# Optimization experiments

Hardware: AMD Instinct MI355X
Metric: run time of the kernel (lower is better)

## Reference

```python
import jax, jax.numpy as jnp
import numpy as np

B, L, H, S2V = 32, 1024, 256, 256
STEP = 1          # HP_SLSTM_step window size
EPS = 1e-3        # LayerNorm eps (added to std, torch-style unbiased std)
NUM_LAYERS = 4
# LayerNorm param row indices in ln_a/ln_b:
# 0..5 -> word gates f1,f2,f3,f4,i,o ; 6 gd ; 7 go ; 8 gf ; 9 gi ; 10 gg


def _ln(x, a, b):
    # torch LayerNorm variant: unbiased std, eps added to std (not var)
    mean = x.mean(-1, keepdims=True)
    d = x - mean
    std = jnp.sqrt((d * d).sum(-1, keepdims=True) / (x.shape[-1] - 1))
    return a * d / (std + EPS) + b


def setup_inputs() -> dict:
    key = jax.random.key(0)
    ks = jax.random.split(key, 16)
    p = lambda k, shp: 0.1 * jax.random.normal(k, shp, dtype=jnp.float32)
    return {
        "word_inputs": jax.random.normal(ks[0], (B, L, H), dtype=jnp.float32),
        "sent_embeddings": jax.random.normal(ks[1], (B, S2V), dtype=jnp.float32),
        "mask": jnp.ones((B, L), dtype=jnp.float32),
        "h0": jax.random.uniform(ks[2], (B, L, H), minval=-0.05, maxval=0.05, dtype=jnp.float32),
        "c0": jax.random.uniform(ks[3], (B, L, H), minval=-0.05, maxval=0.05, dtype=jnp.float32),
        "Wx_g": p(ks[4], (6, H, H)),
        "Wh_g": p(ks[5], (6, 2 * H, H)),
        "Wi_g": p(ks[6], (6, H, H)),
        "Wd_g": p(ks[7], (6, H, H)),
        "b_g": p(ks[8], (6, H)),
        "gWx": p(ks[9], (4, H, H)),   # dummy gates d,i,o,f
        "gWh": p(ks[10], (4, H, H)),
        "gWg": p(ks[11], (4, S2V, H)),  # d,i,o,g
        "gb": p(ks[12], (4, H)),
        "ln_a": jnp.ones((11, H), dtype=jnp.float32),
        "ln_b": jnp.zeros((11, H), dtype=jnp.float32),
        "num_layers": NUM_LAYERS,
    }


def _win_sums(t):
    # sum of left-shifted (before) and right-shifted (after) neighbor states
    bef = jnp.zeros_like(t)
    aft = jnp.zeros_like(t)
    for s in range(1, STEP + 1):
        bef = bef + jnp.pad(t[:, :-s], ((0, 0), (s, 0), (0, 0)))
        aft = aft + jnp.pad(t[:, s:], ((0, 0), (0, s), (0, 0)))
    return bef.reshape(-1, t.shape[-1]), aft.reshape(-1, t.shape[-1])


def reference(word_inputs, sent_embeddings, mask, h0, c0, Wx_g, Wh_g, Wi_g,
              Wd_g, b_g, gWx, gWh, gWg, gb, ln_a, ln_b, num_layers):
    Bs, Ls, Hs = word_inputs.shape
    seq_mask = mask[..., None]                      # (B,L,1)
    msm = (mask * 1e25 - 1e25)[..., None]           # softmax mask (B,L,1)
    emb_h = (word_inputs * seq_mask).reshape(-1, Hs)  # fixed word embedding states
    emb_c = emb_h
    h = h0 * seq_mask
    c = c0 * seq_mask
    dh = h.mean(axis=1)                             # dummy (sentence) node (B,H)
    dc = c.mean(axis=1)

    for _ in range(num_layers):
        comb = h.mean(axis=1)                       # (B,H)
        rh = h.reshape(-1, Hs)                      # (B*L,H)
        tdh = (dh[:, None, :] * seq_mask).reshape(-1, Hs)
        tdc = (dc[:, None, :] * seq_mask).reshape(-1, Hs)

        # --- dummy (sentence-level) node gates ---
        gd = jax.nn.sigmoid(_ln(dh @ gWx[0] + sent_embeddings @ gWg[0] + comb @ gWh[0] + gb[0], ln_a[6], ln_b[6]))
        gi = jax.nn.sigmoid(_ln(dh @ gWx[1] + sent_embeddings @ gWg[1] + comb @ gWh[1], ln_a[9], ln_b[9]) + gb[1])  # bias outside LN, as in source
        gg = sent_embeddings @ gWg[3]
        go = jax.nn.sigmoid(_ln(dh @ gWx[2] + sent_embeddings @ gWg[2] + comb @ gWh[2] + gb[2], ln_a[7], ln_b[7]))
        gf = jax.nn.sigmoid(_ln(tdh @ gWx[3] + rh @ gWh[3] + gb[3], ln_a[8], ln_b[8]))
        gf = gf.reshape(Bs, Ls, Hs) + msm
        scores = jax.nn.softmax(jnp.concatenate([gf, gd[:, None, :], gi[:, None, :]], axis=1), axis=1)
        f_w = scores[:, :Ls]
        d_w = scores[:, Ls]
        i_w = scores[:, Ls + 1]
        dc_new = jnp.sum(f_w * c, axis=1) + d_w * dc + i_w * jnp.tanh(_ln(gg, ln_a[10], ln_b[10]))
        dh_new = go * jnp.tanh(dc_new)

        # --- word node gates (windowed message passing) ---
        hb, ha = _win_sums(h)
        cb, ca = _win_sums(c)
        cat_h = jnp.concatenate([hb, ha], axis=1)   # (B*L, 2H)
        pre = (jnp.einsum('nh,ghk->gnk', emb_h, Wx_g)
               + jnp.einsum('nc,gck->gnk', cat_h, Wh_g)
               + jnp.einsum('nh,ghk->gnk', rh, Wi_g)
               + jnp.einsum('nh,ghk->gnk', tdh, Wd_g)
               + b_g[:, None, :])                   # (6, B*L, H)
        gates = jax.nn.sigmoid(_ln(pre, ln_a[:6, None, :], ln_b[:6, None, :]))
        five = jax.nn.softmax(gates[:5], axis=0)    # normalize f1..f4,i
        f1, f2, f3, f4, i_t = five
        o_t = gates[5]
        c_new = cb * f1 + ca * f2 + emb_c * f3 + tdc * f4 + c.reshape(-1, Hs) * i_t
        h_new = o_t * jnp.tanh(c_new)
        h = h_new.reshape(Bs, Ls, Hs) * seq_mask
        c = c_new.reshape(Bs, Ls, Hs) * seq_mask
        dh, dc = dh_new, dc_new
    return h
```

## Files before the change

### kernel.cpp

```cpp
#include <hip/hip_runtime.h>
#include <cstddef>

#define Bz 32
#define Lz 1024
#define Hz 256
#define Nz (Bz*Lz)
#define NHz ((size_t)Nz*Hz)
#define BHz (Bz*Hz)
#define EPSz 1e-3f
#define NLAYERS 4
#define NCH 64
#define NTC 112
#define CHR 16384

typedef __bf16 bf8_t __attribute__((ext_vector_type(8)));
typedef __bf16 bf4_t __attribute__((ext_vector_type(4)));
typedef float  f4_t  __attribute__((ext_vector_type(4)));

__device__ inline float sigmoidf(float x){ return 1.f/(1.f+expf(-x)); }
__device__ inline float fsig(float x){ return __builtin_amdgcn_rcpf(1.f + __expf(-x)); }
__device__ inline float ftanh(float x){ return 1.f - 2.f*__builtin_amdgcn_rcpf(__expf(2.f*x)+1.f); }

template<int C>
__device__ inline float dppadd(float v){
  int t = __builtin_amdgcn_update_dpp(0, __builtin_bit_cast(int, v), C, 0xf, 0xf, true);
  return v + __builtin_bit_cast(float, t);
}
__device__ inline float dppsum16(float v){
  v = dppadd<0x111>(v);
  v = dppadd<0x112>(v);
  v = dppadd<0x114>(v);
  v = dppadd<0x118>(v);
  return v;
}

__device__ inline void gl_lds16(const void* g, void* l){
  __builtin_amdgcn_global_load_lds(
      (const __attribute__((address_space(1))) void*)g,
      (__attribute__((address_space(3))) void*)l, 16, 0, 0);
}

__device__ inline float2 block_sum2(float a, float b, float* red){
  #pragma unroll
  for (int off=32; off; off>>=1){ a += __shfl_down(a,off,64); b += __shfl_down(b,off,64); }
  int w = threadIdx.x>>6;
  __syncthreads();
  if ((threadIdx.x&63)==0){ red[w]=a; red[4+w]=b; }
  __syncthreads();
  return make_float2(red[0]+red[1]+red[2]+red[3], red[4]+red[5]+red[6]+red[7]);
}

__device__ inline float ln_block(float v, const float* la, const float* lb, int t, float* red){
  float2 ss = block_sum2(v, v*v, red);
  float mean = ss.x*(1.f/Hz);
  float var  = (ss.y - (float)Hz*mean*mean)*(1.f/(Hz-1));
  float isd  = 1.f/(sqrtf(fmaxf(var,0.f))+EPSz);
  return la[t]*(v-mean)*isd + lb[t];
}

__global__ void k_initb(const float* __restrict__ word, const float* __restrict__ h0,
                        const float* __restrict__ c0, const float* __restrict__ mask,
                        __bf16* __restrict__ xe, __bf16* __restrict__ h, __bf16* __restrict__ c){
  int tid = blockIdx.x*256 + threadIdx.x;
  int n = tid >> 5; int c8 = (tid & 31)*8;
  float m = mask[n];
  size_t off = (size_t)n*Hz + c8;
  const float4* wv = (const float4*)(word + off);
  float4 w0 = wv[0], w1 = wv[1];
  bf8_t o;
  o[0]=(__bf16)(w0.x*m); o[1]=(__bf16)(w0.y*m); o[2]=(__bf16)(w0.z*m); o[3]=(__bf16)(w0.w*m);
  o[4]=(__bf16)(w1.x*m); o[5]=(__bf16)(w1.y*m); o[6]=(__bf16)(w1.z*m); o[7]=(__bf16)(w1.w*m);
  *(bf8_t*)(xe + off) = o;
  const float4* hv = (const float4*)(h0 + off);
  float4 a0 = hv[0], a1 = hv[1];
  o[0]=(__bf16)(a0.x*m); o[1]=(__bf16)(a0.y*m); o[2]=(__bf16)(a0.z*m); o[3]=(__bf16)(a0.w*m);
  o[4]=(__bf16)(a1.x*m); o[5]=(__bf16)(a1.y*m); o[6]=(__bf16)(a1.z*m); o[7]=(__bf16)(a1.w*m);
  *(bf8_t*)(h + off) = o;
  const float4* cv = (const float4*)(c0 + off);
  float4 b0 = cv[0], b1 = cv[1];
  o[0]=(__bf16)(b0.x*m); o[1]=(__bf16)(b0.y*m); o[2]=(__bf16)(b0.z*m); o[3]=(__bf16)(b0.w*m);
  o[4]=(__bf16)(b1.x*m); o[5]=(__bf16)(b1.y*m); o[6]=(__bf16)(b1.z*m); o[7]=(__bf16)(b1.w*m);
  *(bf8_t*)(c + off) = o;
}

__global__ void k_packWt(const float* __restrict__ Wx, const float* __restrict__ Wh,
                         const float* __restrict__ Wi, const float* __restrict__ gWh3,
                         __bf16* __restrict__ Wt, __bf16* __restrict__ zbuf){
  int tid = blockIdx.x*256 + threadIdx.x;
  if (tid < 128) zbuf[tid] = (__bf16)0.f;
  int col = tid >> 7;
  int k0  = (tid & 127) << 3;
  if (col >= 1792) return;
  int g = col >> 8, cg = col & 255;
  int seg = k0 >> 8, kl0 = k0 & 255;
  bf8_t o;
  #pragma unroll
  for (int j=0;j<8;j++){
    int kl = kl0 + j;
    float v = 0.f;
    if (g < 6){
      if (seg==0)      v = Wx[((size_t)g*256 + kl)*256 + cg];
      else if (seg==1) v = Wh[((size_t)g*512 + kl)*256 + cg];
      else if (seg==2) v = Wh[((size_t)g*512 + 256 + kl)*256 + cg];
      else             v = Wi[((size_t)g*256 + kl)*256 + cg];
    } else {
      if (seg==3)      v = gWh3[(size_t)kl*256 + cg];
    }
    o[j] = (__bf16)v;
  }
  *(bf8_t*)(Wt + (size_t)col*1024 + k0) = o;
}

__global__ void k_meanpb(const __bf16* __restrict__ x, float* __restrict__ part){
  int b = blockIdx.x, ch = blockIdx.y, t = threadIdx.x;
  const __bf16* p = x + ((size_t)b*Lz + ch*128)*Hz + t;
  float s = 0.f;
  #pragma unroll 4
  for (int l=0;l<128;l++) s += (float)p[(size_t)l*Hz];
  part[(b*8+ch)*Hz + t] = s;
}
__global__ void k_comb8(const float* __restrict__ part, float* __restrict__ o){
  int b = blockIdx.x, t = threadIdx.x;
  float s = 0.f;
  #pragma unroll
  for (int ch=0;ch<8;ch++) s += part[(b*8+ch)*Hz + t];
  o[b*Hz+t] = s*(1.f/Lz);
}

__global__ __launch_bounds__(256) void k_small(
    const float* __restrict__ dh, const float* __restrict__ comb, const float* __restrict__ sent,
    const float* __restrict__ gWx, const float* __restrict__ gWh, const float* __restrict__ gWg,
    const float* __restrict__ gb, const float* __restrict__ Wd_g,
    const float* __restrict__ ln_a, const float* __restrict__ ln_b,
    float* __restrict__ gd, float* __restrict__ gi, float* __restrict__ go,
    float* __restrict__ tgg, float* __restrict__ dhWd7){
  int b = blockIdx.x, which = blockIdx.y, t = threadIdx.x;
  __shared__ float sdh[Hz], sse[Hz], sco[Hz];
  __shared__ float red[8];
  sdh[t]=dh[b*Hz+t]; sse[t]=sent[b*Hz+t]; sco[t]=comb[b*Hz+t];
  __syncthreads();
  float acc=0.f;
  if (which < 3){
    const float* W0 = gWx + which*Hz*Hz;
    const float* W1 = gWg + which*Hz*Hz;
    const float* W2 = gWh + which*Hz*Hz;
    for (int k=0;k<Hz;k++) acc += sdh[k]*W0[k*Hz+t] + sse[k]*W1[k*Hz+t] + sco[k]*W2[k*Hz+t];
    if (which==0){
      float r = ln_block(acc + gb[0*Hz+t], ln_a+6*Hz, ln_b+6*Hz, t, red);
      gd[b*Hz+t] = sigmoidf(r);
    } else if (which==1){
      float r = ln_block(acc, ln_a+9*Hz, ln_b+9*Hz, t, red);
      gi[b*Hz+t] = sigmoidf(r + gb[1*Hz+t]);
    } else {
      float r = ln_block(acc + gb[2*Hz+t], ln_a+7*Hz, ln_b+7*Hz, t, red);
      go[b*Hz+t] = sigmoidf(r);
    }
  } else if (which == 3){
    const float* W = gWg + 3*Hz*Hz;
    for (int k=0;k<Hz;k++) acc += sse[k]*W[k*Hz+t];
    float r = ln_block(acc, ln_a+10*Hz, ln_b+10*Hz, t, red);
    tgg[b*Hz+t] = tanhf(r);
  } else if (which == 4){
    const float* W = gWx + 3*Hz*Hz;
    for (int k=0;k<Hz;k++) acc += sdh[k]*W[k*Hz+t];
    dhWd7[(6*Bz + b)*Hz + t] = acc;
  } else {
    int g = which-5;
    const float* W = Wd_g + g*Hz*Hz;
    for (int k=0;k<Hz;k++) acc += sdh[k]*W[k*Hz+t];
    dhWd7[(g*Bz + b)*Hz + t] = acc;
  }
}

__global__ __launch_bounds__(512) void k_gemm(
    const __bf16* __restrict__ xe, const __bf16* __restrict__ h,
    const __bf16* __restrict__ Wt, const __bf16* __restrict__ zbuf,
    __bf16* __restrict__ pre, int n_base){
  __shared__ __align__(16) __bf16 sA[2][256*64];
  __shared__ __align__(16) __bf16 sB[2][256*64];
  int t = threadIdx.x;
  int w = t>>6, lane = t&63;
  int m16 = lane&15, p = lane>>4;
  int bx = blockIdx.x, by = blockIdx.y;
  int row0 = n_base + bx*256;
  int coltile = by*256;

  f4_t acc[8][4];
  #pragma unroll
  for (int i=0;i<8;i++)
    #pragma unroll
    for (int j=0;j<4;j++) acc[i][j] = (f4_t){0.f,0.f,0.f,0.f};

  int srr = t>>3;
  int sck = t&7;
  int arow = (w>>2)*128 + m16;
  int brow = (w&3)*64 + m16;
  int swz  = m16 & 7;

  auto STAGE = [&](int kt, int buf){
    int seg = kt>>2;
    int kloc = (kt&3)*64;
    #pragma unroll
    for (int it=0; it<4; ++it){
      int drow = it*64 + srr;
      int sc = (sck ^ (drow&7)) << 3;
      int r = row0 + drow;
      const __bf16* asrc;
      if (seg==0)      asrc = xe + (size_t)r*Hz + kloc + sc;
      else if (seg==3) asrc = h + (size_t)r*Hz + kloc + sc;
      else if (seg==1) asrc = ((r&1023)==0)    ? zbuf : h + ((size_t)(r-1)*Hz + kloc + sc);
      else             asrc = ((r&1023)==1023) ? zbuf : h + ((size_t)(r+1)*Hz + kloc + sc);
      gl_lds16(asrc, &sA[buf][drow*64 + sck*8]);
      const __bf16* bsrc = Wt + (size_t)(coltile + drow)*1024 + seg*256 + kloc + sc;
      gl_lds16(bsrc, &sB[buf][drow*64 + sck*8]);
    }
  };

  int kt_s = (by==6) ? 12 : 0;
  STAGE(kt_s, 0);
  __syncthreads();
  int cur = 0;
  #pragma unroll 1
  for (int kt=kt_s; kt<16; ++kt){
    if (kt < 15) STAGE(kt+1, cur^1);
    const char* Ab = (const char*)sA[cur];
    const char* Bb = (const char*)sB[cur];
    bf8_t bb[4][2];
    #pragma unroll
    for (int tc=0;tc<4;tc++)
      #pragma unroll
      for (int kb=0;kb<2;kb++){
        int cofs = ((kb*4 + p) ^ swz) << 4;
        bb[tc][kb] = *(const bf8_t*)(Bb + (brow + tc*16)*128 + cofs);
      }
    #pragma unroll
    for (int q=0; q<4; ++q){
      bf8_t a[2][2];
      #pragma unroll
      for (int i=0;i<2;i++)
        #pragma unroll
        for (int kb=0;kb<2;kb++){
          int cofs = ((kb*4 + p) ^ swz) << 4;
          a[i][kb] = *(const bf8_t*)(Ab + (arow + (q*2+i)*16)*128 + cofs);
        }
      __builtin_amdgcn_s_setprio(1);
      #pragma unroll
      for (int i=0;i<2;i++)
        #pragma unroll
        for (int tc=0;tc<4;tc++)
          #pragma unroll
          for (int kb=0;kb<2;kb++)
            acc[q*2+i][tc] = __builtin_amdgcn_mfma_f32_16x16x32_bf16(a[i][kb], bb[tc][kb], acc[q*2+i][tc], 0, 0, 0);
      __builtin_amdgcn_s_setprio(0);
    }
    __syncthreads();
    cur ^= 1;
  }

  int trg0 = (bx*256 + (w>>2)*128) >> 4;
  int tcg0 = (coltile + (w&3)*64) >> 4;
  #pragma unroll
  for (int tr=0;tr<8;tr++){
    #pragma unroll
    for (int tc=0;tc<4;tc++){
      size_t tile = (size_t)(trg0+tr)*NTC + (tcg0+tc);
      bf4_t o;
      o[0]=(__bf16)acc[tr][tc][0]; o[1]=(__bf16)acc[tr][tc][1];
      o[2]=(__bf16)acc[tr][tc][2]; o[3]=(__bf16)acc[tr][tc][3];
      *(bf4_t*)(pre + tile*256 + lane*4) = o;
    }
  }
}

__global__ __launch_bounds__(1024) void k_epi(
    const __bf16* __restrict__ pre, const __bf16* __restrict__ xe,
    const __bf16* __restrict__ cc, const float* __restrict__ mask,
    const float* __restrict__ dhWd7, const float* __restrict__ b_g,
    const float* __restrict__ gb3, const float* __restrict__ ln_a, const float* __restrict__ ln_b,
    const float* __restrict__ dc,
    float* __restrict__ outf, __bf16* __restrict__ hn, __bf16* __restrict__ cn,
    float* __restrict__ pm, float* __restrict__ ps, float* __restrict__ pn,
    int n_base, int last){
  __shared__ float sred_s[16][7][16];
  __shared__ float sred_q[16][7][16];
  __shared__ float smean[7][16];
  __shared__ float sisd[7][16];
  __shared__ float hsh[16*260];
  int t = threadIdx.x;
  int n0 = n_base + blockIdx.x*16;
  int b = n0 >> 10;
  int w16 = t>>6, lane = t&63, m16 = lane&15, p = lane>>4;
  int col = w16*16 + m16;
  size_t trk = blockIdx.x;

  bf4_t pv[7];
  float wd[7], bg[7], la[7], lb[7];
  #pragma unroll
  for (int g=0; g<7; ++g){
    size_t tile = trk*NTC + g*16 + w16;
    pv[g] = *(const bf4_t*)(pre + tile*256 + lane*4);
    wd[g] = dhWd7[(g*Bz + b)*Hz + col];
    bg[g] = (g<6) ? b_g[g*Hz + col] : gb3[col];
    int lnr = (g<6) ? g : 8;
    la[g] = ln_a[lnr*Hz+col]; lb[g] = ln_b[lnr*Hz+col];
  }
  float msk4[4], cvv[4], cb4[4], ca4[4], em4[4];
  #pragma unroll
  for (int reg=0; reg<4; ++reg){
    int n2 = n0 + p*4 + reg;
    int l2 = n2 & 1023;
    msk4[reg] = mask[n2];
    cvv[reg] = (float)cc[(size_t)n2*Hz + col];
    cb4[reg] = (l2==0)    ? 0.f : (float)cc[(size_t)(n2-1)*Hz + col];
    ca4[reg] = (l2==1023) ? 0.f : (float)cc[(size_t)(n2+1)*Hz + col];
    em4[reg] = (float)xe[(size_t)n2*Hz + col];
  }
  float tdc = dc[b*Hz + col];

  float acc[7][4];
  #pragma unroll
  for (int g=0; g<7; ++g){
    float s_r[4], q_r[4];
    #pragma unroll
    for (int reg=0; reg<4; ++reg){
      float x = (float)pv[g][reg] + msk4[reg]*wd[g] + bg[g];
      acc[g][reg] = x;
      s_r[reg] = dppsum16(x);
      q_r[reg] = dppsum16(x*x);
    }
    if (m16==15){
      #pragma unroll
      for (int reg=0; reg<4; ++reg){
        sred_s[w16][g][p*4+reg] = s_r[reg];
        sred_q[w16][g][p*4+reg] = q_r[reg];
      }
    }
  }
  __syncthreads();

  if (t < 112){
    int g = t>>4, row = t&15;
    float ss=0.f, qq=0.f;
    #pragma unroll
    for (int ww=0; ww<16; ++ww){
      ss += sred_s[ww][g][row];
      qq += sred_q[ww][g][row];
    }
    float mean = ss*(1.f/Hz);
    float var  = (qq - (float)Hz*mean*mean)*(1.f/(Hz-1));
    smean[g][row] = mean;
    sisd[g][row]  = __builtin_amdgcn_rcpf(sqrtf(fmaxf(var,0.f))+EPSz);
  }
  __syncthreads();

  #pragma unroll
  for (int g=0; g<7; ++g){
    #pragma unroll
    for (int reg=0; reg<4; ++reg){
      int row = p*4+reg;
      acc[g][reg] = fsig(la[g]*(acc[g][reg]-smean[g][row])*sisd[g][row] + lb[g]);
    }
  }

  {
    float mm = -1e30f, gfv[4];
    #pragma unroll
    for (int reg=0; reg<4; ++reg){
      float gv = acc[6][reg] + (msk4[reg]*1e25f - 1e25f);
      gfv[reg] = gv;
      mm = fmaxf(mm, gv);
    }
    float ss=0.f, nn=0.f;
    #pragma unroll
    for (int reg=0; reg<4; ++reg){
      float e = __expf(gfv[reg]-mm);
      ss += e; nn += e*cvv[reg];
    }
    #pragma unroll
    for (int off=16; off<64; off<<=1){
      float mo = __shfl_xor(mm, off, 64);
      float so = __shfl_xor(ss, off, 64);
      float no = __shfl_xor(nn, off, 64);
      float mN = fmaxf(mm, mo);
      float ea = __expf(mm-mN), eb = __expf(mo-mN);
      ss = ss*ea + so*eb; nn = nn*ea + no*eb; mm = mN;
    }
    if (p==0){
      int ch = (n0 >> 4) & (NCH-1);
      int idx = (b*NCH + ch)*Hz + col;
      pm[idx]=mm; ps[idx]=ss; pn[idx]=nn;
    }
  }

  float cnv[4];
  #pragma unroll
  for (int reg=0; reg<4; ++reg){
    float msk = msk4[reg];
    float g0=acc[0][reg], g1=acc[1][reg], g2=acc[2][reg], g3=acc[3][reg], g4=acc[4][reg];
    float m5 = fmaxf(fmaxf(fmaxf(g0,g1),fmaxf(g2,g3)),g4);
    float e0=__expf(g0-m5), e1=__expf(g1-m5), e2=__expf(g2-m5), e3=__expf(g3-m5), e4=__expf(g4-m5);
    float inv = __builtin_amdgcn_rcpf(e0+e1+e2+e3+e4);
    float cnew = (cb4[reg]*e0 + ca4[reg]*e1 + em4[reg]*e2 + (tdc*msk)*e3 + cvv[reg]*e4)*inv;
    float hv = acc[5][reg]*ftanh(cnew);
    hsh[(p*4+reg)*260 + col] = hv*msk;
    cnv[reg] = cnew*msk;
  }
  __syncthreads();
  {
    int row = t>>6, c4 = lane*4;
    int n = n0 + row;
    const float* src = hsh + row*260 + c4;
    float v0=src[0], v1=src[1], v2=src[2], v3=src[3];
    if (last){
      *(float4*)(outf + (size_t)n*Hz + c4) = make_float4(v0,v1,v2,v3);
    } else {
      bf4_t o; o[0]=(__bf16)v0; o[1]=(__bf16)v1; o[2]=(__bf16)v2; o[3]=(__bf16)v3;
      *(bf4_t*)(hn + (size_t)n*Hz + c4) = o;
    }
  }
  __syncthreads();
  #pragma unroll
  for (int reg=0; reg<4; ++reg) hsh[(p*4+reg)*260 + col] = cnv[reg];
  __syncthreads();
  {
    int row = t>>6, c4 = lane*4;
    const float* src = hsh + row*260 + c4;
    bf4_t o; o[0]=(__bf16)src[0]; o[1]=(__bf16)src[1]; o[2]=(__bf16)src[2]; o[3]=(__bf16)src[3];
    *(bf4_t*)(cn + (size_t)(n0+row)*Hz + c4) = o;
  }
}

__global__ void k_soft_comb(const float* __restrict__ pm, const float* __restrict__ ps,
    const float* __restrict__ pn,
    const float* __restrict__ gd, const float* __restrict__ gi, const float* __restrict__ go,
    const float* __restrict__ tgg, const float* __restrict__ dc,
    float* __restrict__ dc_new, float* __restrict__ dh_new){
  int b = blockIdx.x, t = threadIdx.x;
  float vgd = gd[b*Hz+t], vgi = gi[b*Hz+t];
  float m = fmaxf(vgd, vgi);
  for (int ch=0; ch<NCH; ch++) m = fmaxf(m, pm[(b*NCH+ch)*Hz + t]);
  float ed = expf(vgd - m), ei = expf(vgi - m);
  float s  = ed + ei;
  float num = ed*dc[b*Hz+t] + ei*tgg[b*Hz+t];
  for (int ch=0; ch<NCH; ch++){
    int idx = (b*NCH+ch)*Hz + t;
    float e = expf(pm[idx] - m);
    s   += ps[idx]*e;
    num += pn[idx]*e;
  }
  float dcn = num/s;
  dc_new[b*Hz+t] = dcn;
  dh_new[b*Hz+t] = go[b*Hz+t]*tanhf(dcn);
}

extern "C" void kernel_launch(void* const* d_in, const int* in_sizes, int n_in,
                              void* d_out, int out_size, void* d_ws, size_t ws_size,
                              hipStream_t stream) {
  const float* word  = (const float*)d_in[0];
  const float* sent  = (const float*)d_in[1];
  const float* mask  = (const float*)d_in[2];
  const float* h0    = (const float*)d_in[3];
  const float* c0    = (const float*)d_in[4];
  const float* Wx_g  = (const float*)d_in[5];
  const float* Wh_g  = (const float*)d_in[6];
  const float* Wi_g  = (const float*)d_in[7];
  const float* Wd_g  = (const float*)d_in[8];
  const float* b_g   = (const float*)d_in[9];
  const float* gWx   = (const float*)d_in[10];
  const float* gWh   = (const float*)d_in[11];
  const float* gWg   = (const float*)d_in[12];
  const float* gb    = (const float*)d_in[13];
  const float* ln_a  = (const float*)d_in[14];
  const float* ln_b  = (const float*)d_in[15];
  float* out = (float*)d_out;

  char* wc = (char*)d_ws;
  __bf16* xe  = (__bf16*)wc;  wc += NHz*2;
  __bf16* h_a = (__bf16*)wc;  wc += NHz*2;
  __bf16* h_b = (__bf16*)wc;  wc += NHz*2;
  __bf16* c_a = (__bf16*)wc;  wc += NHz*2;
  __bf16* c_b = (__bf16*)wc;  wc += NHz*2;
  __bf16* pre = (__bf16*)wc;  wc += (size_t)(CHR/16)*NTC*256*2;
  __bf16* Wt  = (__bf16*)wc;  wc += (size_t)1792*1024*2;
  __bf16* zbuf = (__bf16*)wc; wc += 256;
  float* dh_a = (float*)wc;   wc += BHz*4;
  float* dh_b = (float*)wc;   wc += BHz*4;
  float* dc_a = (float*)wc;   wc += BHz*4;
  float* dc_b = (float*)wc;   wc += BHz*4;
  float* comb = (float*)wc;   wc += BHz*4;
  float* gd   = (float*)wc;   wc += BHz*4;
  float* gi_  = (float*)wc;   wc += BHz*4;
  float* go_  = (float*)wc;   wc += BHz*4;
  float* tgg  = (float*)wc;   wc += BHz*4;
  float* dhWd7 = (float*)wc;  wc += 7*BHz*4;
  float* pmean = (float*)wc;  wc += 8*BHz*4;
  float* pm = (float*)wc;     wc += (size_t)Bz*NCH*Hz*4;
  float* ps = (float*)wc;     wc += (size_t)Bz*NCH*Hz*4;
  float* pn = (float*)wc;     wc += (size_t)Bz*NCH*Hz*4;

  k_packWt<<<896, 256, 0, stream>>>(Wx_g, Wh_g, Wi_g, gWh + 3*Hz*Hz, Wt, zbuf);
  k_initb<<<4096, 256, 0, stream>>>(word, h0, c0, mask, xe, h_a, c_a);
  k_meanpb<<<dim3(Bz,8), 256, 0, stream>>>(h_a, pmean);
  k_comb8<<<Bz, 256, 0, stream>>>(pmean, dh_a);
  k_meanpb<<<dim3(Bz,8), 256, 0, stream>>>(c_a, pmean);
  k_comb8<<<Bz, 256, 0, stream>>>(pmean, dc_a);

  __bf16* hc=h_a; __bf16* hn=h_b;
  __bf16* cc=c_a; __bf16* cn=c_b;
  float* dhc=dh_a; float* dcc=dc_a; float* dhn=dh_b; float* dcn=dc_b;

  for (int layer=0; layer<NLAYERS; ++layer){
    k_meanpb<<<dim3(Bz,8), 256, 0, stream>>>(hc, pmean);
    k_comb8<<<Bz, 256, 0, stream>>>(pmean, comb);
    k_small<<<dim3(Bz,11), 256, 0, stream>>>(dhc, comb, sent, gWx, gWh, gWg, gb, Wd_g,
                                             ln_a, ln_b, gd, gi_, go_, tgg, dhWd7);
    int last = (layer == NLAYERS-1) ? 1 : 0;
    for (int chunk=0; chunk<Nz/CHR; ++chunk){
      int n_base = chunk*CHR;
      k_gemm<<<dim3(CHR/256, 7), 512, 0, stream>>>(xe, hc, Wt, zbuf, pre, n_base);
      k_epi<<<CHR/16, 1024, 0, stream>>>(pre, xe, cc, mask, dhWd7, b_g, gb + 3*Hz,
                                         ln_a, ln_b, dcc, out, hn, cn, pm, ps, pn,
                                         n_base, last);
    }
    k_soft_comb<<<Bz, 256, 0, stream>>>(pm, ps, pn, gd, gi_, go_, tgg, dcc, dcn, dhn);
    __bf16* tb;
    tb=hc; hc=hn; hn=tb;
    tb=cc; cc=cn; cn=tb;
    float* tmp;
    tmp=dhc; dhc=dhn; dhn=tmp;
    tmp=dcc; dcc=dcn; dcn=tmp;
  }
  (void)in_sizes; (void)n_in; (void)out_size; (void)ws_size;
}
```

Before: 1.409 ms.

## Interleave next-tile staging with MFMA sub-steps using split loads and barriers

Splits the prefetch of the next K tile into four quarters (two for weights, two for activations), issued one per MFMA sub-step, and moves the B-fragment LDS reads inside the first sub-step. Explicit s_barrier/sched_barrier pairs around each MFMA group replace the single end-of-iteration __syncthreads, with an explicit vmcnt(0) wait before swapping buffers. The goal is to spread global-to-LDS traffic across compute so the memory and matrix units overlap. The cost is many more workgroup barriers per iteration, which may stall waves.

```diff
diff --git a/kernel.cpp b/kernel.cpp
--- a/kernel.cpp
+++ b/kernel.cpp
@@ -191,48 +191,46 @@
     #pragma unroll
     for (int j=0;j<4;j++) acc[i][j] = (f4_t){0.f,0.f,0.f,0.f};
 
-  int srr = t>>3;
-  int sck = t&7;
   int arow = (w>>2)*128 + m16;
   int brow = (w&3)*64 + m16;
   int swz  = m16 & 7;
 
-  auto STAGE = [&](int kt, int buf){
-    int seg = kt>>2;
-    int kloc = (kt&3)*64;
-    #pragma unroll
-    for (int it=0; it<4; ++it){
-      int drow = it*64 + srr;
+  int srr = t>>3;
+  int sck = t&7;
+
+  auto STAGE_HALF = [&](int kt, int half, int buf){
+    int seg = kt>>2, kloc = (kt&3)*64;
+    #pragma unroll
+    for (int it=0; it<2; ++it){
+      int drow = (half&1)*128 + it*64 + srr;
       int sc = (sck ^ (drow&7)) << 3;
-      int r = row0 + drow;
-      const __bf16* asrc;
-      if (seg==0)      asrc = xe + (size_t)r*Hz + kloc + sc;
-      else if (seg==3) asrc = h + (size_t)r*Hz + kloc + sc;
-      else if (seg==1) asrc = ((r&1023)==0)    ? zbuf : h + ((size_t)(r-1)*Hz + kloc + sc);
-      else             asrc = ((r&1023)==1023) ? zbuf : h + ((size_t)(r+1)*Hz + kloc + sc);
-      gl_lds16(asrc, &sA[buf][drow*64 + sck*8]);
-      const __bf16* bsrc = Wt + (size_t)(coltile + drow)*1024 + seg*256 + kloc + sc;
-      gl_lds16(bsrc, &sB[buf][drow*64 + sck*8]);
+      if (half < 2){
+        const __bf16* bsrc = Wt + (size_t)(coltile + drow)*1024 + seg*256 + kloc + sc;
+        gl_lds16(bsrc, &sB[buf][drow*64 + sck*8]);
+      } else {
+        int r = row0 + drow;
+        const __bf16* asrc;
+        if (seg==0)      asrc = xe + (size_t)r*Hz + kloc + sc;
+        else if (seg==3) asrc = h + (size_t)r*Hz + kloc + sc;
+        else if (seg==1) asrc = ((r&1023)==0)    ? zbuf : h + ((size_t)(r-1)*Hz + kloc + sc);
+        else             asrc = ((r&1023)==1023) ? zbuf : h + ((size_t)(r+1)*Hz + kloc + sc);
+        gl_lds16(asrc, &sA[buf][drow*64 + sck*8]);
+      }
     }
   };
 
   int kt_s = (by==6) ? 12 : 0;
-  STAGE(kt_s, 0);
-  __syncthreads();
+  STAGE_HALF(kt_s,0,0); STAGE_HALF(kt_s,1,0);
+  STAGE_HALF(kt_s,2,0); STAGE_HALF(kt_s,3,0);
+  asm volatile("s_waitcnt vmcnt(0)" ::: "memory");
+  __builtin_amdgcn_s_barrier();
+
   int cur = 0;
   #pragma unroll 1
   for (int kt=kt_s; kt<16; ++kt){
-    if (kt < 15) STAGE(kt+1, cur^1);
     const char* Ab = (const char*)sA[cur];
     const char* Bb = (const char*)sB[cur];
     bf8_t bb[4][2];
-    #pragma unroll
-    for (int tc=0;tc<4;tc++)
-      #pragma unroll
-      for (int kb=0;kb<2;kb++){
-        int cofs = ((kb*4 + p) ^ swz) << 4;
-        bb[tc][kb] = *(const bf8_t*)(Bb + (brow + tc*16)*128 + cofs);
-      }
     #pragma unroll
     for (int q=0; q<4; ++q){
       bf8_t a[2][2];
@@ -243,6 +241,19 @@
           int cofs = ((kb*4 + p) ^ swz) << 4;
           a[i][kb] = *(const bf8_t*)(Ab + (arow + (q*2+i)*16)*128 + cofs);
         }
+      if (q==0){
+        #pragma unroll
+        for (int tc=0;tc<4;tc++)
+          #pragma unroll
+          for (int kb=0;kb<2;kb++){
+            int cofs = ((kb*4 + p) ^ swz) << 4;
+            bb[tc][kb] = *(const bf8_t*)(Bb + (brow + tc*16)*128 + cofs);
+          }
+      }
+      if (kt < 15) STAGE_HALF(kt+1, q, cur^1);
+      __builtin_amdgcn_sched_barrier(0);
+      __builtin_amdgcn_s_barrier();
+      __builtin_amdgcn_sched_barrier(0);
       __builtin_amdgcn_s_setprio(1);
       #pragma unroll
       for (int i=0;i<2;i++)
@@ -252,8 +263,16 @@
           for (int kb=0;kb<2;kb++)
             acc[q*2+i][tc] = __builtin_amdgcn_mfma_f32_16x16x32_bf16(a[i][kb], bb[tc][kb], acc[q*2+i][tc], 0, 0, 0);
       __builtin_amdgcn_s_setprio(0);
-    }
-    __syncthreads();
+      __builtin_amdgcn_sched_barrier(0);
+      __builtin_amdgcn_s_barrier();
+      __builtin_amdgcn_sched_barrier(0);
+    }
+    if (kt < 15){
+      asm volatile("s_waitcnt vmcnt(0)" ::: "memory");
+      __builtin_amdgcn_sched_barrier(0);
+      __builtin_amdgcn_s_barrier();
+      __builtin_amdgcn_sched_barrier(0);
+    }
     cur ^= 1;
   }
 
```

Measured after the change: 1.391 ms. Within noise of the previous version (-1.2%).
